# Kernel tuning notes

Measured on AMD Instinct MI355X. Metric: run time of the kernel, lower is better.

## Reference

```python
import jax, jax.numpy as jnp
import numpy as np

THETA = 10000.0

def _rope_cos_sin(seq_len, head_dim, dtype=jnp.float32):
    # matches precompute_freqs_cis: freqs over even indices of head_dim
    inv = 1.0 / (THETA ** (jnp.arange(0, head_dim, 2, dtype=jnp.float32) / head_dim))  # [hd/2]
    ang = jnp.arange(seq_len, dtype=jnp.float32)[:, None] * inv[None, :]               # [S, hd/2]
    return jnp.cos(ang).astype(dtype), jnp.sin(ang).astype(dtype)

def _apply_rope(x, cos, sin):
    # x: [b, h, s, d]; pairs are interleaved (d r) with r=2 -> complex (even=real, odd=imag)
    xe = x[..., 0::2]
    xo = x[..., 1::2]
    re = xe * cos - xo * sin
    im = xe * sin + xo * cos
    # interleave back: [..., d/2, 2] -> [..., d]
    return jnp.stack([re, im], axis=-1).reshape(x.shape)

def setup_inputs() -> dict:
    key = jax.random.key(0)
    ks = jax.random.split(key, 8)
    B, S, D = 2, 2048, 1024
    s = 0.02
    return {
        "query": jax.random.normal(ks[0], (B, S, D), jnp.float32),
        "key": jax.random.normal(ks[1], (B, S, D), jnp.float32),
        "value": jax.random.normal(ks[2], (B, S, D), jnp.float32),
        "q_w": jax.random.normal(ks[3], (D, D), jnp.float32) * s,
        "q_b": jnp.zeros((D,), jnp.float32),
        "k_w": jax.random.normal(ks[4], (D, D), jnp.float32) * s,
        "k_b": jnp.zeros((D,), jnp.float32),
        "v_w": jax.random.normal(ks[5], (D, D), jnp.float32) * s,
        "v_b": jnp.zeros((D,), jnp.float32),
        "o_w": jax.random.normal(ks[6], (D, D), jnp.float32) * s,
        "o_b": jnp.zeros((D,), jnp.float32),
    }

def reference(query, key, value, q_w, q_b, k_w, k_b, v_w, v_b, o_w, o_b):
    H = 16
    B, S, D = query.shape
    hd = D // H
    scaling = hd ** -0.5

    def split_heads(x):  # [b, s, (h d)] -> [b, h, s, d]
        return x.reshape(B, -1, H, hd).transpose(0, 2, 1, 3)

    q = split_heads(query @ q_w.T + q_b)
    k = split_heads(key @ k_w.T + k_b)
    v = split_heads(value @ v_w.T + v_b)

    cos, sin = _rope_cos_sin(S, hd)
    q = _apply_rope(q, cos, sin)
    k = _apply_rope(k, cos, sin)

    scores = jnp.einsum('bhqd,bhkd->bhqk', q, k) * scaling  # [B,H,S,S]
    attn = jax.nn.softmax(scores, axis=-1)
    out = jnp.einsum('bhqk,bhkd->bhqd', attn, v)            # [B,H,S,hd]
    out = out.transpose(0, 2, 1, 3).reshape(B, S, D)
    return out @ o_w.T + o_b
```

## Files before the change

### kernel.cpp

```cpp
#include <hip/hip_runtime.h>
#include <math.h>

#define B_  2
#define S_  2048
#define D_  1024
#define H_  16
#define HD_ 64
#define M_  (B_*S_)

typedef __attribute__((ext_vector_type(8))) short bf16x8;
typedef __attribute__((ext_vector_type(4))) short bf16x4;
typedef __attribute__((ext_vector_type(4))) float f32x4;
typedef unsigned short ushort_t;

#define MFMA32 __builtin_amdgcn_mfma_f32_16x16x32_bf16
#define MFMA16 __builtin_amdgcn_mfma_f32_16x16x16bf16_1k

__device__ inline unsigned short f2bf(float x) {
    unsigned u = __float_as_uint(x);
    unsigned r = (u + 0x7fff + ((u >> 16) & 1)) >> 16;
    return (unsigned short)r;
}
__device__ inline void gload16(const ushort_t* g, ushort_t* l) {
    __builtin_amdgcn_global_load_lds(
        (const __attribute__((address_space(1))) unsigned*)g,
        (__attribute__((address_space(3))) unsigned*)l, 16, 0, 0);
}

__global__ void rope_table_kernel(float* __restrict__ cost, float* __restrict__ sint) {
    int tid = blockIdx.x * blockDim.x + threadIdx.x;
    int s = tid >> 5;
    int i = tid & 31;
    double inv = pow(10000.0, -((double)(2 * i) / (double)HD_));
    double ang = (double)s * inv;
    cost[tid] = (float)cos(ang);
    sint[tid] = (float)sin(ang);
}

__global__ __launch_bounds__(256) void conv3(
    const float* __restrict__ s0, ushort_t* __restrict__ d0,
    const float* __restrict__ s1, ushort_t* __restrict__ d1,
    const float* __restrict__ s2, ushort_t* __restrict__ d2, int n4)
{
    int z = blockIdx.y;
    const float* in = z == 0 ? s0 : z == 1 ? s1 : s2;
    ushort_t* dst   = z == 0 ? d0 : z == 1 ? d1 : d2;
    int i = blockIdx.x * 256 + threadIdx.x;
    if (i >= n4) return;
    float4 v = ((const float4*)in)[i];
    unsigned short h0 = f2bf(v.x), h1 = f2bf(v.y), h2 = f2bf(v.z), h3 = f2bf(v.w);
    ((uint2*)dst)[i] = make_uint2((unsigned)h0 | ((unsigned)h1 << 16),
                                  (unsigned)h2 | ((unsigned)h3 << 16));
}
__global__ __launch_bounds__(256) void conv4(
    const float* __restrict__ s0, ushort_t* __restrict__ d0,
    const float* __restrict__ s1, ushort_t* __restrict__ d1,
    const float* __restrict__ s2, ushort_t* __restrict__ d2,
    const float* __restrict__ s3, ushort_t* __restrict__ d3, int n4)
{
    int z = blockIdx.y;
    const float* in = z == 0 ? s0 : z == 1 ? s1 : z == 2 ? s2 : s3;
    ushort_t* dst   = z == 0 ? d0 : z == 1 ? d1 : z == 2 ? d2 : d3;
    int i = blockIdx.x * 256 + threadIdx.x;
    if (i >= n4) return;
    float4 v = ((const float4*)in)[i];
    unsigned short h0 = f2bf(v.x), h1 = f2bf(v.y), h2 = f2bf(v.z), h3 = f2bf(v.w);
    ((uint2*)dst)[i] = make_uint2((unsigned)h0 | ((unsigned)h1 << 16),
                                  (unsigned)h2 | ((unsigned)h3 << 16));
}

__global__ __launch_bounds__(256, 4) void fused_qkv(
    const ushort_t* __restrict__ A0, const ushort_t* __restrict__ A1,
    const ushort_t* __restrict__ A2,
    const ushort_t* __restrict__ W0, const ushort_t* __restrict__ W1,
    const ushort_t* __restrict__ W2,
    const float* __restrict__ b0, const float* __restrict__ b1,
    const float* __restrict__ b2,
    ushort_t* __restrict__ O0, ushort_t* __restrict__ O1,
    ushort_t* __restrict__ O2,
    const float* __restrict__ cost, const float* __restrict__ sint)
{
    __shared__ ushort_t Ab[4096];
    __shared__ ushort_t Wb[4096];

    const int tid  = threadIdx.x;
    const int wq   = tid >> 6;
    const int lane = tid & 63;
    const int l16  = lane & 15;
    const int quad = lane >> 4;
    const int bm   = blockIdx.y * 128;
    const int bn   = blockIdx.x * 128;
    const int z    = blockIdx.z;

    const ushort_t* A = z == 0 ? A0 : z == 1 ? A1 : A2;
    const ushort_t* W = z == 0 ? W0 : z == 1 ? W1 : W2;
    const float* bias = z == 0 ? b0 : z == 1 ? b1 : b2;

    const int m16 = tid & 15;
    const int akq = (tid >> 4) & 3;
    const int tw  = tid >> 6;

    const ushort_t* gA0 = A + (size_t)(bm + tw * 16 + m16) * D_ + akq * 8;
    const ushort_t* gA1 = gA0 + (size_t)64 * D_;
    const ushort_t* gW0 = W + (size_t)(bn + tw * 16 + m16) * D_ + akq * 8;
    const ushort_t* gW1 = gW0 + (size_t)64 * D_;

    ushort_t* lA0 = &Ab[tw * 512];
    ushort_t* lA1 = &Ab[(tw + 4) * 512];
    ushort_t* lW0 = &Wb[tw * 512];
    ushort_t* lW1 = &Wb[(tw + 4) * 512];

    const int wm = wq >> 1, wn = wq & 1;

    f32x4 acc[4][4];
#pragma unroll
    for (int mt = 0; mt < 4; ++mt)
#pragma unroll
        for (int nt = 0; nt < 4; ++nt)
            acc[mt][nt] = (f32x4){0.f, 0.f, 0.f, 0.f};

    for (int k0 = 0; k0 < D_; k0 += 32) {
        __syncthreads();
        gload16(gA0 + k0, lA0);
        gload16(gA1 + k0, lA1);
        gload16(gW0 + k0, lW0);
        gload16(gW1 + k0, lW1);
        __syncthreads();

        bf16x8 af[4], wf[4];
#pragma unroll
        for (int mt = 0; mt < 4; ++mt)
            af[mt] = *(const bf16x8*)&Ab[(wm * 4 + mt) * 512 + lane * 8];
#pragma unroll
        for (int nt = 0; nt < 4; ++nt)
            wf[nt] = *(const bf16x8*)&Wb[(wn * 4 + nt) * 512 + lane * 8];
#pragma unroll
        for (int mt = 0; mt < 4; ++mt)
#pragma unroll
            for (int nt = 0; nt < 4; ++nt)
                acc[mt][nt] = MFMA32(af[mt], wf[nt], acc[mt][nt], 0, 0, 0);
    }

    if (z == 0) {
        const float scale = 0.18033688011112042f;
#pragma unroll
        for (int mt = 0; mt < 4; ++mt) {
            int m = bm + wm * 64 + mt * 16 + quad * 4;
#pragma unroll
            for (int nt = 0; nt < 4; ++nt) {
                int n = bn + wn * 64 + nt * 16 + l16;
                float bb = bias[n];
                int h = n >> 6, d = n & 63, p = d >> 1;
#pragma unroll
                for (int r = 0; r < 4; ++r) {
                    int mm = m + r;
                    int s = mm & (S_ - 1), b = mm >> 11;
                    float x = acc[mt][nt][r] + bb;
                    float cs = cost[s * 32 + p], sn = sint[s * 32 + p];
                    float part = __shfl_xor(x, 1);
                    float y = (d & 1) ? (part * sn + x * cs)
                                      : (x * cs - part * sn);
                    O0[((size_t)(b * H_ + h) * S_ + s) * HD_ + d] = f2bf(y * scale);
                }
            }
        }
    } else if (z == 1) {
#pragma unroll
        for (int mt = 0; mt < 4; ++mt) {
            int m = bm + wm * 64 + mt * 16 + quad * 4;
#pragma unroll
            for (int nt = 0; nt < 4; ++nt) {
                int n = bn + wn * 64 + nt * 16 + l16;
                float bb = bias[n];
                int h = n >> 6, d = n & 63, p = d >> 1;
                int sub = ((d >> 5) & 1);
                int dq  = (d >> 3) & 3;
                int dj  = d & 7;
#pragma unroll
                for (int r = 0; r < 4; ++r) {
                    int mm = m + r;
                    int s = mm & (S_ - 1), b = mm >> 11;
                    float x = acc[mt][nt][r] + bb;
                    float cs = cost[s * 32 + p], sn = sint[s * 32 + p];
                    float part = __shfl_xor(x, 1);
                    float y = (d & 1) ? (part * sn + x * cs)
                                      : (x * cs - part * sn);
                    int kt  = s >> 5;
                    int st  = ((s >> 4) & 1) * 2 + sub;
                    size_t idx = ((size_t)(b * H_ + h) * 64 + kt) * 2048
                               + st * 512 + dq * 128 + (s & 15) * 8 + dj;
                    O1[idx] = f2bf(y);
                }
            }
        }
    } else {
#pragma unroll
        for (int mt = 0; mt < 4; ++mt) {
            int m = bm + wm * 64 + mt * 16 + quad * 4;
            int b = m >> 11, s0 = m & (S_ - 1);
            int vt = s0 >> 5;
            int kk = s0 & 31;
            int keyp = ((kk & 15) >> 2) * 8 + ((kk >> 4) & 1) * 4;
#pragma unroll
            for (int nt = 0; nt < 4; ++nt) {
                int n = bn + wn * 64 + nt * 16 + l16;
                float bb = bias[n];
                int h = n >> 6, d = n & 63;
                int mtv = d >> 4, dd = d & 15;
                unsigned short hh[4];
#pragma unroll
                for (int r = 0; r < 4; ++r)
                    hh[r] = f2bf(acc[mt][nt][r] + bb);
                size_t idx = ((size_t)(b * H_ + h) * 64 + vt) * 2048
                           + mtv * 512 + dd * 32 + keyp;
                *(uint2*)(O2 + idx) = make_uint2(
                    (unsigned)hh[0] | ((unsigned)hh[1] << 16),
                    (unsigned)hh[2] | ((unsigned)hh[3] << 16));
            }
        }
    }
}

__global__ __launch_bounds__(256, 4) void proj_o(
    const ushort_t* __restrict__ A, const ushort_t* __restrict__ W,
    const float* __restrict__ bias, float* __restrict__ outf)
{
    __shared__ ushort_t Ab[2048];
    __shared__ ushort_t Wb[4096];

    const int tid  = threadIdx.x;
    const int wq   = tid >> 6;
    const int lane = tid & 63;
    const int l16  = lane & 15;
    const int quad = lane >> 4;
    const int bm   = blockIdx.y * 64;
    const int bn   = blockIdx.x * 128;

    const int m16 = tid & 15;
    const int akq = (tid >> 4) & 3;
    const int tw  = tid >> 6;

    const ushort_t* gA  = A + (size_t)(bm + tw * 16 + m16) * D_ + akq * 8;
    const ushort_t* gW0 = W + (size_t)(bn + tw * 16 + m16) * D_ + akq * 8;
    const ushort_t* gW1 = gW0 + (size_t)64 * D_;

    ushort_t* lA  = &Ab[tw * 512];
    ushort_t* lW0 = &Wb[tw * 512];
    ushort_t* lW1 = &Wb[(tw + 4) * 512];

    const int wm = wq >> 1, wn = wq & 1;

    f32x4 acc[2][4];
#pragma unroll
    for (int mt = 0; mt < 2; ++mt)
#pragma unroll
        for (int nt = 0; nt < 4; ++nt)
            acc[mt][nt] = (f32x4){0.f, 0.f, 0.f, 0.f};

    for (int k0 = 0; k0 < D_; k0 += 32) {
        __syncthreads();
        gload16(gA + k0, lA);
        gload16(gW0 + k0, lW0);
        gload16(gW1 + k0, lW1);
        __syncthreads();

        bf16x8 af[2], wf[4];
#pragma unroll
        for (int mt = 0; mt < 2; ++mt)
            af[mt] = *(const bf16x8*)&Ab[(wm * 2 + mt) * 512 + lane * 8];
#pragma unroll
        for (int nt = 0; nt < 4; ++nt)
            wf[nt] = *(const bf16x8*)&Wb[(wn * 4 + nt) * 512 + lane * 8];
#pragma unroll
        for (int mt = 0; mt < 2; ++mt)
#pragma unroll
            for (int nt = 0; nt < 4; ++nt)
                acc[mt][nt] = MFMA32(af[mt], wf[nt], acc[mt][nt], 0, 0, 0);
    }

#pragma unroll
    for (int mt = 0; mt < 2; ++mt) {
        int m = bm + wm * 32 + mt * 16 + quad * 4;
#pragma unroll
        for (int nt = 0; nt < 4; ++nt) {
            int n = bn + wn * 64 + nt * 16 + l16;
            float bb = bias[n];
#pragma unroll
            for (int r = 0; r < 4; ++r)
                outf[(size_t)(m + r) * D_ + n] = acc[mt][nt][r] + bb;
        }
    }
}

__global__ __launch_bounds__(256, 4) void attn_mfma(
    const ushort_t* __restrict__ Q, const ushort_t* __restrict__ Kf,
    const ushort_t* __restrict__ Vf, ushort_t* __restrict__ AO)
{
    __shared__ ushort_t KS[4096];
    __shared__ ushort_t VS[4096];
    __shared__ float    MRG[2 * 64 * 33];
    __shared__ float    PSB[2 * 64 * 2];

    const int tid  = threadIdx.x;
    const int wq   = tid >> 6;
    const int lane = tid & 63;
    const int l16  = lane & 15;
    const int quad = lane >> 4;
    const int qg   = wq & 1;
    const int ks   = wq >> 1;
    const int bh   = blockIdx.y;
    const int q0   = blockIdx.x * 64 + qg * 32;

    bf16x8 qa[2][2];
#pragma unroll
    for (int nh = 0; nh < 2; ++nh)
#pragma unroll
        for (int c = 0; c < 2; ++c) {
            int row = q0 + nh * 16 + l16;
            qa[nh][c] = *(const bf16x8*)(Q + ((size_t)bh * S_ + row) * HD_
                                           + c * 32 + quad * 8);
        }

    f32x4 oacc[2][4];
#pragma unroll
    for (int nh = 0; nh < 2; ++nh)
#pragma unroll
        for (int mt = 0; mt < 4; ++mt)
            oacc[nh][mt] = (f32x4){0.f, 0.f, 0.f, 0.f};
    float ps[2] = {0.f, 0.f};

    const ushort_t* Kp = Kf + (size_t)bh * 64 * 2048;
    const ushort_t* Vp = Vf + (size_t)bh * 64 * 2048;
    const ushort_t* Kc = KS + ks * 2048;
    const ushort_t* Vc = VS + ks * 2048;

    for (int i = 0; i < 32; ++i) {
        __syncthreads();
        gload16(Kp + tid * 8,        KS + tid * 8);
        gload16(Kp + 2048 + tid * 8, KS + 2048 + tid * 8);
        gload16(Vp + tid * 8,        VS + tid * 8);
        gload16(Vp + 2048 + tid * 8, VS + 2048 + tid * 8);
        Kp += 4096; Vp += 4096;
        __syncthreads();

        f32x4 s[2][2];
#pragma unroll
        for (int nh = 0; nh < 2; ++nh)
#pragma unroll
            for (int g = 0; g < 2; ++g)
                s[nh][g] = (f32x4){0.f, 0.f, 0.f, 0.f};
#pragma unroll
        for (int c = 0; c < 2; ++c) {
            bf16x8 k0 = *(const bf16x8*)&Kc[(0 + c) * 512 + lane * 8];
            bf16x8 k1 = *(const bf16x8*)&Kc[(2 + c) * 512 + lane * 8];
            s[0][0] = MFMA32(k0, qa[0][c], s[0][0], 0, 0, 0);
            s[0][1] = MFMA32(k1, qa[0][c], s[0][1], 0, 0, 0);
            s[1][0] = MFMA32(k0, qa[1][c], s[1][0], 0, 0, 0);
            s[1][1] = MFMA32(k1, qa[1][c], s[1][1], 0, 0, 0);
        }

        bf16x4 pb[2][2];
#pragma unroll
        for (int nh = 0; nh < 2; ++nh)
#pragma unroll
            for (int g = 0; g < 2; ++g) {
                float p0 = __builtin_exp2f(s[nh][g][0]);
                float p1 = __builtin_exp2f(s[nh][g][1]);
                float p2 = __builtin_exp2f(s[nh][g][2]);
                float p3 = __builtin_exp2f(s[nh][g][3]);
                ps[nh] += (p0 + p1) + (p2 + p3);
                union { bf16x4 v; unsigned u[2]; } t;
                t.u[0] = __builtin_amdgcn_perm(__float_as_uint(p1),
                                               __float_as_uint(p0), 0x07060302);
                t.u[1] = __builtin_amdgcn_perm(__float_as_uint(p3),
                                               __float_as_uint(p2), 0x07060302);
                pb[nh][g] = t.v;
            }

#pragma unroll
        for (int mt = 0; mt < 4; ++mt) {
            bf16x8 vv = *(const bf16x8*)&Vc[mt * 512 + l16 * 32 + quad * 8];
            bf16x4 v0 = __builtin_shufflevector(vv, vv, 0, 1, 2, 3);
            bf16x4 v1 = __builtin_shufflevector(vv, vv, 4, 5, 6, 7);
            oacc[0][mt] = MFMA16(v0, pb[0][0], oacc[0][mt], 0, 0, 0);
            oacc[0][mt] = MFMA16(v1, pb[0][1], oacc[0][mt], 0, 0, 0);
            oacc[1][mt] = MFMA16(v0, pb[1][0], oacc[1][mt], 0, 0, 0);
            oacc[1][mt] = MFMA16(v1, pb[1][1], oacc[1][mt], 0, 0, 0);
        }
    }

    if (ks == 1) {
        float* mr = &MRG[(qg * 64 + lane) * 33];
#pragma unroll
        for (int nh = 0; nh < 2; ++nh)
#pragma unroll
            for (int mt = 0; mt < 4; ++mt)
#pragma unroll
                for (int r = 0; r < 4; ++r)
                    mr[nh * 16 + mt * 4 + r] = oacc[nh][mt][r];
        PSB[(qg * 64 + lane) * 2 + 0] = ps[0];
        PSB[(qg * 64 + lane) * 2 + 1] = ps[1];
    }
    __syncthreads();
    if (ks == 0) {
        const float* mr = &MRG[(qg * 64 + lane) * 33];
#pragma unroll
        for (int nh = 0; nh < 2; ++nh)
#pragma unroll
            for (int mt = 0; mt < 4; ++mt)
#pragma unroll
                for (int r = 0; r < 4; ++r)
                    oacc[nh][mt][r] += mr[nh * 16 + mt * 4 + r];
        ps[0] += PSB[(qg * 64 + lane) * 2 + 0];
        ps[1] += PSB[(qg * 64 + lane) * 2 + 1];
#pragma unroll
        for (int nh = 0; nh < 2; ++nh) {
            ps[nh] += __shfl_xor(ps[nh], 16);
            ps[nh] += __shfl_xor(ps[nh], 32);
        }
        const int b = bh >> 4, h = bh & 15;
#pragma unroll
        for (int nh = 0; nh < 2; ++nh) {
            float inv = 1.0f / ps[nh];
            int q = q0 + nh * 16 + l16;
#pragma unroll
            for (int mt = 0; mt < 4; ++mt) {
                unsigned short hh[4];
#pragma unroll
                for (int r = 0; r < 4; ++r)
                    hh[r] = f2bf(oacc[nh][mt][r] * inv);
                size_t base = ((size_t)b * S_ + q) * D_ + h * HD_
                            + mt * 16 + quad * 4;
                *(uint2*)(AO + base) = make_uint2(
                    (unsigned)hh[0] | ((unsigned)hh[1] << 16),
                    (unsigned)hh[2] | ((unsigned)hh[3] << 16));
            }
        }
    }
}

extern "C" void kernel_launch(void* const* d_in, const int* in_sizes, int n_in,
                              void* d_out, int out_size, void* d_ws, size_t ws_size,
                              hipStream_t stream) {
    const float* query = (const float*)d_in[0];
    const float* key   = (const float*)d_in[1];
    const float* value = (const float*)d_in[2];
    const float* q_w   = (const float*)d_in[3];
    const float* q_b   = (const float*)d_in[4];
    const float* k_w   = (const float*)d_in[5];
    const float* k_b   = (const float*)d_in[6];
    const float* v_w   = (const float*)d_in[7];
    const float* v_b   = (const float*)d_in[8];
    const float* o_w   = (const float*)d_in[9];
    const float* o_b   = (const float*)d_in[10];
    float* out = (float*)d_out;

    const size_t NT = (size_t)M_ * D_;
    const size_t WT = (size_t)D_ * D_;
    ushort_t* p = (ushort_t*)d_ws;
    ushort_t* qa_b = p; p += NT;
    ushort_t* ka_b = p; p += NT;
    ushort_t* va_b = p; p += NT;
    ushort_t* wqb  = p; p += WT;
    ushort_t* wkb  = p; p += WT;
    ushort_t* wvb  = p; p += WT;
    ushort_t* wob  = p; p += WT;
    ushort_t* Qb   = p; p += NT;
    ushort_t* Kfr  = p; p += NT;
    ushort_t* Vfr  = p; p += NT;
    ushort_t* AO   = p; p += NT;
    float* cost = (float*)p;
    float* sint = cost + (size_t)S_ * 32;

    rope_table_kernel<<<(S_ * 32) / 256, 256, 0, stream>>>(cost, sint);

    dim3 gc_a((unsigned)(NT / 4 / 256), 3);
    conv3<<<gc_a, 256, 0, stream>>>(query, qa_b, key, ka_b, value, va_b,
                                    (int)(NT / 4));
    dim3 gc_w((unsigned)(WT / 4 / 256), 4);
    conv4<<<gc_w, 256, 0, stream>>>(q_w, wqb, k_w, wkb, v_w, wvb, o_w, wob,
                                    (int)(WT / 4));

    dim3 gq(D_ / 128, M_ / 128, 3);
    fused_qkv<<<gq, 256, 0, stream>>>(
        qa_b, ka_b, va_b, wqb, wkb, wvb,
        q_b, k_b, v_b, Qb, Kfr, Vfr, cost, sint);

    dim3 agrid(S_ / 64, B_ * H_);
    attn_mfma<<<agrid, 256, 0, stream>>>(Qb, Kfr, Vfr, AO);

    dim3 go(D_ / 128, M_ / 64);
    proj_o<<<go, 256, 0, stream>>>(AO, wob, o_b, out);
}
```

Measured before the change: 260.3 us.

## Enlarge attention query tile, compute row sums via MFMA, merge prep kernels

The attention kernel now processes 128 queries per block (64 per wave) instead of 64, so each K/V tile loaded into LDS is reused across twice as many query rows. Softmax row sums move from scalar adds and shuffles to an MFMA against a ones vector. The V fragment layout is changed to a contiguous per-lane load, with the QKV epilogue writing V in the matching order. The three preprocessing launches (rope table and bf16 conversions) are folded into one kernel. The larger tile roughly doubles accumulator registers, so launch bounds drop to 2 waves and the grid halves, which lowers occupancy and parallelism.

```diff
diff --git a/kernel.cpp b/kernel.cpp
--- a/kernel.cpp
+++ b/kernel.cpp
@@ -27,41 +27,40 @@
         (__attribute__((address_space(3))) unsigned*)l, 16, 0, 0);
 }
 
-__global__ void rope_table_kernel(float* __restrict__ cost, float* __restrict__ sint) {
-    int tid = blockIdx.x * blockDim.x + threadIdx.x;
-    int s = tid >> 5;
-    int i = tid & 31;
-    double inv = pow(10000.0, -((double)(2 * i) / (double)HD_));
-    double ang = (double)s * inv;
-    cost[tid] = (float)cos(ang);
-    sint[tid] = (float)sin(ang);
-}
-
-__global__ __launch_bounds__(256) void conv3(
-    const float* __restrict__ s0, ushort_t* __restrict__ d0,
-    const float* __restrict__ s1, ushort_t* __restrict__ d1,
-    const float* __restrict__ s2, ushort_t* __restrict__ d2, int n4)
+__global__ __launch_bounds__(256) void prep(
+    const float* __restrict__ qa, const float* __restrict__ ka,
+    const float* __restrict__ va,
+    const float* __restrict__ qw, const float* __restrict__ kw,
+    const float* __restrict__ vw, const float* __restrict__ ow,
+    ushort_t* __restrict__ qab, ushort_t* __restrict__ kab,
+    ushort_t* __restrict__ vab,
+    ushort_t* __restrict__ qwb, ushort_t* __restrict__ kwb,
+    ushort_t* __restrict__ vwb, ushort_t* __restrict__ owb,
+    float* __restrict__ cost, float* __restrict__ sint)
 {
-    int z = blockIdx.y;
-    const float* in = z == 0 ? s0 : z == 1 ? s1 : s2;
-    ushort_t* dst   = z == 0 ? d0 : z == 1 ? d1 : d2;
-    int i = blockIdx.x * 256 + threadIdx.x;
-    if (i >= n4) return;
-    float4 v = ((const float4*)in)[i];
-    unsigned short h0 = f2bf(v.x), h1 = f2bf(v.y), h2 = f2bf(v.z), h3 = f2bf(v.w);
-    ((uint2*)dst)[i] = make_uint2((unsigned)h0 | ((unsigned)h1 << 16),
-                                  (unsigned)h2 | ((unsigned)h3 << 16));
-}
-__global__ __launch_bounds__(256) void conv4(
-    const float* __restrict__ s0, ushort_t* __restrict__ d0,
-    const float* __restrict__ s1, ushort_t* __restrict__ d1,
-    const float* __restrict__ s2, ushort_t* __restrict__ d2,
-    const float* __restrict__ s3, ushort_t* __restrict__ d3, int n4)
-{
-    int z = blockIdx.y;
-    const float* in = z == 0 ? s0 : z == 1 ? s1 : z == 2 ? s2 : s3;
-    ushort_t* dst   = z == 0 ? d0 : z == 1 ? d1 : z == 2 ? d2 : d3;
-    int i = blockIdx.x * 256 + threadIdx.x;
+    const int z = blockIdx.y;
+    const int i = blockIdx.x * 256 + threadIdx.x;
+    if (z == 7) {
+        if (blockIdx.x >= (S_ * 32) / 256) return;
+        int s = i >> 5, w = i & 31;
+        double inv = pow(10000.0, -((double)(2 * w) / (double)HD_));
+        double ang = (double)s * inv;
+        cost[i] = (float)cos(ang);
+        sint[i] = (float)sin(ang);
+        return;
+    }
+    const float* in;
+    ushort_t* dst;
+    int n4;
+    switch (z) {
+        case 0: in = qa; dst = qab; n4 = (M_ * D_) / 4; break;
+        case 1: in = ka; dst = kab; n4 = (M_ * D_) / 4; break;
+        case 2: in = va; dst = vab; n4 = (M_ * D_) / 4; break;
+        case 3: in = qw; dst = qwb; n4 = (D_ * D_) / 4; break;
+        case 4: in = kw; dst = kwb; n4 = (D_ * D_) / 4; break;
+        case 5: in = vw; dst = vwb; n4 = (D_ * D_) / 4; break;
+        default: in = ow; dst = owb; n4 = (D_ * D_) / 4; break;
+    }
     if (i >= n4) return;
     float4 v = ((const float4*)in)[i];
     unsigned short h0 = f2bf(v.x), h1 = f2bf(v.y), h2 = f2bf(v.z), h3 = f2bf(v.w);
@@ -200,7 +199,8 @@
             int b = m >> 11, s0 = m & (S_ - 1);
             int vt = s0 >> 5;
             int kk = s0 & 31;
-            int keyp = ((kk & 15) >> 2) * 8 + ((kk >> 4) & 1) * 4;
+            int qd = (kk & 15) >> 2;
+            int w0 = ((kk >> 4) & 1) * 4;
 #pragma unroll
             for (int nt = 0; nt < 4; ++nt) {
                 int n = bn + wn * 64 + nt * 16 + l16;
@@ -212,7 +212,7 @@
                 for (int r = 0; r < 4; ++r)
                     hh[r] = f2bf(acc[mt][nt][r] + bb);
                 size_t idx = ((size_t)(b * H_ + h) * 64 + vt) * 2048
-                           + mtv * 512 + dd * 32 + keyp;
+                           + mtv * 512 + qd * 128 + dd * 8 + w0;
                 *(uint2*)(O2 + idx) = make_uint2(
                     (unsigned)hh[0] | ((unsigned)hh[1] << 16),
                     (unsigned)hh[2] | ((unsigned)hh[3] << 16));
@@ -292,14 +292,14 @@
     }
 }
 
-__global__ __launch_bounds__(256, 4) void attn_mfma(
+__global__ __launch_bounds__(256, 2) void attn_mfma(
     const ushort_t* __restrict__ Q, const ushort_t* __restrict__ Kf,
     const ushort_t* __restrict__ Vf, ushort_t* __restrict__ AO)
 {
     __shared__ ushort_t KS[4096];
     __shared__ ushort_t VS[4096];
-    __shared__ float    MRG[2 * 64 * 33];
-    __shared__ float    PSB[2 * 64 * 2];
+    __shared__ float    MRG[128 * 65];
+    __shared__ float    PSB[128];
 
     const int tid  = threadIdx.x;
     const int wq   = tid >> 6;
@@ -309,11 +309,11 @@
     const int qg   = wq & 1;
     const int ks   = wq >> 1;
     const int bh   = blockIdx.y;
-    const int q0   = blockIdx.x * 64 + qg * 32;
-
-    bf16x8 qa[2][2];
-#pragma unroll
-    for (int nh = 0; nh < 2; ++nh)
+    const int q0   = blockIdx.x * 128 + qg * 64;
+
+    bf16x8 qa[4][2];
+#pragma unroll
+    for (int nh = 0; nh < 4; ++nh)
 #pragma unroll
         for (int c = 0; c < 2; ++c) {
             int row = q0 + nh * 16 + l16;
@@ -321,13 +321,18 @@
                                            + c * 32 + quad * 8);
         }
 
-    f32x4 oacc[2][4];
-#pragma unroll
-    for (int nh = 0; nh < 2; ++nh)
+    f32x4 oacc[4][4];
+    f32x4 osum[4];
+#pragma unroll
+    for (int nh = 0; nh < 4; ++nh) {
+        osum[nh] = (f32x4){0.f, 0.f, 0.f, 0.f};
 #pragma unroll
         for (int mt = 0; mt < 4; ++mt)
             oacc[nh][mt] = (f32x4){0.f, 0.f, 0.f, 0.f};
-    float ps[2] = {0.f, 0.f};
+    }
+
+    const bf16x4 ones = {(short)0x3F80, (short)0x3F80,
+                         (short)0x3F80, (short)0x3F80};
 
     const ushort_t* Kp = Kf + (size_t)bh * 64 * 2048;
     const ushort_t* Vp = Vf + (size_t)bh * 64 * 2048;
@@ -343,32 +348,36 @@
         Kp += 4096; Vp += 4096;
         __syncthreads();
 
-        f32x4 s[2][2];
-#pragma unroll
-        for (int nh = 0; nh < 2; ++nh)
+        bf16x8 kf[2][2];
+#pragma unroll
+        for (int g = 0; g < 2; ++g)
+#pragma unroll
+            for (int c = 0; c < 2; ++c)
+                kf[g][c] = *(const bf16x8*)&Kc[(g * 2 + c) * 512 + lane * 8];
+
+        f32x4 s[4][2];
+#pragma unroll
+        for (int nh = 0; nh < 4; ++nh)
 #pragma unroll
             for (int g = 0; g < 2; ++g)
                 s[nh][g] = (f32x4){0.f, 0.f, 0.f, 0.f};
 #pragma unroll
-        for (int c = 0; c < 2; ++c) {
-            bf16x8 k0 = *(const bf16x8*)&Kc[(0 + c) * 512 + lane * 8];
-            bf16x8 k1 = *(const bf16x8*)&Kc[(2 + c) * 512 + lane * 8];
-            s[0][0] = MFMA32(k0, qa[0][c], s[0][0], 0, 0, 0);
-            s[0][1] = MFMA32(k1, qa[0][c], s[0][1], 0, 0, 0);
-            s[1][0] = MFMA32(k0, qa[1][c], s[1][0], 0, 0, 0);
-            s[1][1] = MFMA32(k1, qa[1][c], s[1][1], 0, 0, 0);
-        }
-
-        bf16x4 pb[2][2];
-#pragma unroll
-        for (int nh = 0; nh < 2; ++nh)
+        for (int c = 0; c < 2; ++c)
+#pragma unroll
+            for (int nh = 0; nh < 4; ++nh)
+#pragma unroll
+                for (int g = 0; g < 2; ++g)
+                    s[nh][g] = MFMA32(kf[g][c], qa[nh][c], s[nh][g], 0, 0, 0);
+
+        bf16x4 pb[4][2];
+#pragma unroll
+        for (int nh = 0; nh < 4; ++nh)
 #pragma unroll
             for (int g = 0; g < 2; ++g) {
                 float p0 = __builtin_exp2f(s[nh][g][0]);
                 float p1 = __builtin_exp2f(s[nh][g][1]);
                 float p2 = __builtin_exp2f(s[nh][g][2]);
                 float p3 = __builtin_exp2f(s[nh][g][3]);
-                ps[nh] += (p0 + p1) + (p2 + p3);
                 union { bf16x4 v; unsigned u[2]; } t;
                 t.u[0] = __builtin_amdgcn_perm(__float_as_uint(p1),
                                                __float_as_uint(p0), 0x07060302);
@@ -379,56 +388,52 @@
 
 #pragma unroll
         for (int mt = 0; mt < 4; ++mt) {
-            bf16x8 vv = *(const bf16x8*)&Vc[mt * 512 + l16 * 32 + quad * 8];
+            bf16x8 vv = *(const bf16x8*)&Vc[mt * 512 + lane * 8];
             bf16x4 v0 = __builtin_shufflevector(vv, vv, 0, 1, 2, 3);
             bf16x4 v1 = __builtin_shufflevector(vv, vv, 4, 5, 6, 7);
-            oacc[0][mt] = MFMA16(v0, pb[0][0], oacc[0][mt], 0, 0, 0);
-            oacc[0][mt] = MFMA16(v1, pb[0][1], oacc[0][mt], 0, 0, 0);
-            oacc[1][mt] = MFMA16(v0, pb[1][0], oacc[1][mt], 0, 0, 0);
-            oacc[1][mt] = MFMA16(v1, pb[1][1], oacc[1][mt], 0, 0, 0);
+#pragma unroll
+            for (int nh = 0; nh < 4; ++nh) {
+                oacc[nh][mt] = MFMA16(v0, pb[nh][0], oacc[nh][mt], 0, 0, 0);
+                oacc[nh][mt] = MFMA16(v1, pb[nh][1], oacc[nh][mt], 0, 0, 0);
+            }
+        }
+#pragma unroll
+        for (int nh = 0; nh < 4; ++nh) {
+            osum[nh] = MFMA16(ones, pb[nh][0], osum[nh], 0, 0, 0);
+            osum[nh] = MFMA16(ones, pb[nh][1], osum[nh], 0, 0, 0);
         }
     }
 
     if (ks == 1) {
-        float* mr = &MRG[(qg * 64 + lane) * 33];
-#pragma unroll
-        for (int nh = 0; nh < 2; ++nh)
+#pragma unroll
+        for (int nh = 0; nh < 4; ++nh) {
 #pragma unroll
             for (int mt = 0; mt < 4; ++mt)
 #pragma unroll
                 for (int r = 0; r < 4; ++r)
-                    mr[nh * 16 + mt * 4 + r] = oacc[nh][mt][r];
-        PSB[(qg * 64 + lane) * 2 + 0] = ps[0];
-        PSB[(qg * 64 + lane) * 2 + 1] = ps[1];
+                    MRG[(qg * 64 + nh * 16 + l16) * 65 + mt * 16 + quad * 4 + r]
+                        = oacc[nh][mt][r];
+            if (quad == 0)
+                PSB[qg * 64 + nh * 16 + l16] = osum[nh][0];
+        }
     }
     __syncthreads();
     if (ks == 0) {
-        const float* mr = &MRG[(qg * 64 + lane) * 33];
-#pragma unroll
-        for (int nh = 0; nh < 2; ++nh)
-#pragma unroll
-            for (int mt = 0; mt < 4; ++mt)
-#pragma unroll
-                for (int r = 0; r < 4; ++r)
-                    oacc[nh][mt][r] += mr[nh * 16 + mt * 4 + r];
-        ps[0] += PSB[(qg * 64 + lane) * 2 + 0];
-        ps[1] += PSB[(qg * 64 + lane) * 2 + 1];
-#pragma unroll
-        for (int nh = 0; nh < 2; ++nh) {
-            ps[nh] += __shfl_xor(ps[nh], 16);
-            ps[nh] += __shfl_xor(ps[nh], 32);
-        }
         const int b = bh >> 4, h = bh & 15;
 #pragma unroll
-        for (int nh = 0; nh < 2; ++nh) {
-            float inv = 1.0f / ps[nh];
+        for (int nh = 0; nh < 4; ++nh) {
+            float pst = osum[nh][0] + PSB[qg * 64 + nh * 16 + l16];
+            float inv = 1.0f / pst;
             int q = q0 + nh * 16 + l16;
 #pragma unroll
             for (int mt = 0; mt < 4; ++mt) {
                 unsigned short hh[4];
 #pragma unroll
-                for (int r = 0; r < 4; ++r)
-                    hh[r] = f2bf(oacc[nh][mt][r] * inv);
+                for (int r = 0; r < 4; ++r) {
+                    float x = oacc[nh][mt][r]
+                        + MRG[(qg * 64 + nh * 16 + l16) * 65 + mt * 16 + quad * 4 + r];
+                    hh[r] = f2bf(x * inv);
+                }
                 size_t base = ((size_t)b * S_ + q) * D_ + h * HD_
                             + mt * 16 + quad * 4;
                 *(uint2*)(AO + base) = make_uint2(
@@ -472,21 +477,17 @@
     float* cost = (float*)p;
     float* sint = cost + (size_t)S_ * 32;
 
-    rope_table_kernel<<<(S_ * 32) / 256, 256, 0, stream>>>(cost, sint);
-
-    dim3 gc_a((unsigned)(NT / 4 / 256), 3);
-    conv3<<<gc_a, 256, 0, stream>>>(query, qa_b, key, ka_b, value, va_b,
-                                    (int)(NT / 4));
-    dim3 gc_w((unsigned)(WT / 4 / 256), 4);
-    conv4<<<gc_w, 256, 0, stream>>>(q_w, wqb, k_w, wkb, v_w, wvb, o_w, wob,
-                                    (int)(WT / 4));
+    dim3 gp((unsigned)(NT / 4 / 256), 8);
+    prep<<<gp, 256, 0, stream>>>(query, key, value, q_w, k_w, v_w, o_w,
+                                 qa_b, ka_b, va_b, wqb, wkb, wvb, wob,
+                                 cost, sint);
 
     dim3 gq(D_ / 128, M_ / 128, 3);
     fused_qkv<<<gq, 256, 0, stream>>>(
         qa_b, ka_b, va_b, wqb, wkb, wvb,
         q_b, k_b, v_b, Qb, Kfr, Vfr, cost, sint);
 
-    dim3 agrid(S_ / 64, B_ * H_);
+    dim3 agrid(S_ / 128, B_ * H_);
     attn_mfma<<<agrid, 256, 0, stream>>>(Qb, Kfr, Vfr, AO);
 
     dim3 go(D_ / 128, M_ / 64);
```

Result: no change. 257.4 us (-1.1%).
